# Kernel tuning notes

Hardware: AMD Instinct MI355X
Metric: run time of the kernel (lower is better)

Reference implementation:

```python
import jax, jax.numpy as jnp
import numpy as np

B, T, D = 8, 1024, 1024
H, HD, KVH, R = 16, 64, 4, 256   # heads, head_dim, kv_heads, kv_lora_rank
K = 31                            # depthwise conv kernel
FF = 4 * D
EPS = 1e-5


def _ln(x, g, b):
    m = jnp.mean(x, -1, keepdims=True)
    v = jnp.mean((x - m) ** 2, -1, keepdims=True)
    return (x - m) * jax.lax.rsqrt(v + EPS) * g + b


def _rope_tables(seq, dim):
    inv = 1.0 / (10000.0 ** (np.arange(0, dim, 2, dtype=np.float32) / dim))
    t = np.arange(seq, dtype=np.float32)
    f = np.einsum('i,j->ij', t, inv)
    emb = np.concatenate([f, f], -1)
    return jnp.asarray(np.cos(emb)), jnp.asarray(np.sin(emb))


def _rope(x, cos, sin):
    # x: [B, h, T, HD]; cos/sin: [T, HD]
    x1, x2 = jnp.split(x, 2, axis=-1)
    return x * cos + jnp.concatenate([-x2, x1], -1) * sin


def setup_inputs() -> dict:
    key = jax.random.key(0)
    ks = iter(jax.random.split(key, 48))
    def w(shape, s=0.02):
        return jax.random.normal(next(ks), shape, jnp.float32) * s
    d = {}
    d['x'] = jax.random.normal(next(ks), (B, T, D), jnp.float32)
    d['ff1_ng'] = jnp.ones(D); d['ff1_nb'] = jnp.zeros(D)
    d['ff1_w1'] = w((D, FF)); d['ff1_b1'] = jnp.zeros(FF)
    d['ff1_w2'] = w((FF, D)); d['ff1_b2'] = jnp.zeros(D)
    d['attn_ng'] = jnp.ones(D); d['attn_nb'] = jnp.zeros(D)
    d['wq'] = w((D, H * HD)); d['wkva'] = w((D, R + HD))
    d['kvn_g'] = jnp.ones(R); d['kvn_b'] = jnp.zeros(R)
    d['wkvb'] = w((R, KVH * HD * 2)); d['wo'] = w((H * HD, D))
    d['conv_ng'] = jnp.ones(D); d['conv_nb'] = jnp.zeros(D)
    d['pw1_w'] = w((D, 2 * D)); d['pw1_b'] = jnp.zeros(2 * D)
    d['dw_w'] = w((D, 1, K)); d['dw_b'] = jnp.zeros(D)
    d['bn_g'] = jnp.ones(D); d['bn_b'] = jnp.zeros(D)
    d['bn_rm'] = jnp.zeros(D); d['bn_rv'] = jnp.ones(D)
    d['pw2_w'] = w((D, D)); d['pw2_b'] = jnp.zeros(D)
    d['ff2_ng'] = jnp.ones(D); d['ff2_nb'] = jnp.zeros(D)
    d['ff2_w1'] = w((D, FF)); d['ff2_b1'] = jnp.zeros(FF)
    d['ff2_w2'] = w((FF, D)); d['ff2_b2'] = jnp.zeros(D)
    d['fin_g'] = jnp.ones(D); d['fin_b'] = jnp.zeros(D)
    return d


def _ffn(x, ng, nb, w1, b1, w2, b2):
    h = jax.nn.silu(_ln(x, ng, nb) @ w1 + b1)
    return h @ w2 + b2


def _rmla(x, ng, nb, wq, wkva, kvn_g, kvn_b, wkvb, wo):
    h = _ln(x, ng, nb)
    q = (h @ wq).reshape(B, T, H, HD).transpose(0, 2, 1, 3)
    kva = h @ wkva                                  # [B,T,R+HD]; k_pe part unused (as in source)
    lat = _ln(kva[..., :R], kvn_g, kvn_b)
    kv = lat @ wkvb
    k = kv[..., :KVH * HD].reshape(B, T, KVH, HD).transpose(0, 2, 1, 3)
    v = kv[..., KVH * HD:].reshape(B, T, KVH, HD).transpose(0, 2, 1, 3)
    cos, sin = _rope_tables(T, HD)
    q = _rope(q, cos, sin)
    k = _rope(k, cos, sin)
    g = H // KVH
    k = jnp.repeat(k, g, axis=1)
    v = jnp.repeat(v, g, axis=1)
    s = jnp.einsum('bhqd,bhkd->bhqk', q, k) * (HD ** -0.5)
    a = jax.nn.softmax(s.astype(jnp.float32), axis=-1).astype(q.dtype)
    o = jnp.einsum('bhqk,bhkd->bhqd', a, v)
    o = o.transpose(0, 2, 1, 3).reshape(B, T, H * HD)
    return o @ wo


def _convmod(x, ng, nb, pw1_w, pw1_b, dw_w, dw_b, bn_g, bn_b, bn_rm, bn_rv, pw2_w, pw2_b):
    h = _ln(x, ng, nb)
    h = h @ pw1_w + pw1_b                           # [B,T,2D]
    a, gate = jnp.split(h, 2, axis=-1)
    h = a * jax.nn.sigmoid(gate)                    # GLU over channels
    h = h.transpose(0, 2, 1)                        # [B,D,T]
    h = jax.lax.conv_general_dilated(h, dw_w, (1,), [(K // 2, K // 2)],
                                     dimension_numbers=('NCH', 'OIH', 'NCH'),
                                     feature_group_count=D) + dw_b[None, :, None]
    h = (h - bn_rm[None, :, None]) * jax.lax.rsqrt(bn_rv[None, :, None] + EPS)
    h = h * bn_g[None, :, None] + bn_b[None, :, None]
    h = jax.nn.silu(h)
    h = h.transpose(0, 2, 1)                        # [B,T,D]
    return h @ pw2_w + pw2_b


def reference(x, ff1_ng, ff1_nb, ff1_w1, ff1_b1, ff1_w2, ff1_b2,
              attn_ng, attn_nb, wq, wkva, kvn_g, kvn_b, wkvb, wo,
              conv_ng, conv_nb, pw1_w, pw1_b, dw_w, dw_b, bn_g, bn_b, bn_rm, bn_rv, pw2_w, pw2_b,
              ff2_ng, ff2_nb, ff2_w1, ff2_b1, ff2_w2, ff2_b2, fin_g, fin_b):
    # Conformer block (macaron): half-FF, RMLA attention, gated depthwise conv, half-FF, final LN
    x = x + 0.5 * _ffn(x, ff1_ng, ff1_nb, ff1_w1, ff1_b1, ff1_w2, ff1_b2)
    x = x + _rmla(x, attn_ng, attn_nb, wq, wkva, kvn_g, kvn_b, wkvb, wo)
    x = x + _convmod(x, conv_ng, conv_nb, pw1_w, pw1_b, dw_w, dw_b, bn_g, bn_b, bn_rm, bn_rv, pw2_w, pw2_b)
    x = x + 0.5 * _ffn(x, ff2_ng, ff2_nb, ff2_w1, ff2_b1, ff2_w2, ff2_b2)
    return _ln(x, fin_g, fin_b)
```

## Files before the change

### kernel.cpp

```cpp
#include <hip/hip_runtime.h>
#include <stdint.h>

typedef unsigned short u16;
using bf16x8 = __attribute__((ext_vector_type(8))) __bf16;
using f32x4  = __attribute__((ext_vector_type(4))) float;

__device__ __forceinline__ u16 f2bf(float f) {
    uint32_t u = __float_as_uint(f);
    u += 0x7fffu + ((u >> 16) & 1u);
    return (u16)(u >> 16);
}
__device__ __forceinline__ float bf2f(u16 u) {
    return __uint_as_float(((uint32_t)u) << 16);
}
__device__ __forceinline__ void gload16(const void* g, void* l) {
    __builtin_amdgcn_global_load_lds(
        (__attribute__((address_space(1))) void*)(uintptr_t)g,
        (__attribute__((address_space(3))) void*)(uintptr_t)l,
        16, 0, 0);
}

template <int OUTF32>
__global__ __launch_bounds__(256) void ln_kernel(const float* __restrict__ in,
                                                 const float* __restrict__ g,
                                                 const float* __restrict__ b,
                                                 void* __restrict__ out, int D) {
    const int row = blockIdx.x;
    const int tid = threadIdx.x;
    const float* x = in + (size_t)row * D;
    const int nv = D >> 8;
    float v[4];
    float s1 = 0.f, s2 = 0.f;
    for (int i = 0; i < nv; ++i) {
        float t = x[tid + (i << 8)];
        v[i] = t; s1 += t; s2 += t * t;
    }
    for (int o = 1; o < 64; o <<= 1) {
        s1 += __shfl_xor(s1, o, 64);
        s2 += __shfl_xor(s2, o, 64);
    }
    __shared__ float r1[4], r2[4];
    const int w = tid >> 6;
    if ((tid & 63) == 0) { r1[w] = s1; r2[w] = s2; }
    __syncthreads();
    s1 = r1[0] + r1[1] + r1[2] + r1[3];
    s2 = r2[0] + r2[1] + r2[2] + r2[3];
    const float mean = s1 / (float)D;
    const float var  = s2 / (float)D - mean * mean;
    const float inv  = rsqrtf(var + 1e-5f);
    for (int i = 0; i < nv; ++i) {
        int c = tid + (i << 8);
        float y = (v[i] - mean) * inv * g[c] + b[c];
        if (OUTF32) ((float*)out)[(size_t)row * D + c] = y;
        else        ((u16*)out)[(size_t)row * D + c] = f2bf(y);
    }
}

template <int GLUPERM>
__global__ __launch_bounds__(256) void wconvert_t(const float* __restrict__ W0,
                                                  u16* __restrict__ Wt0,
                                                  const float* __restrict__ W1,
                                                  u16* __restrict__ Wt1,
                                                  int K, int N, int ldw) {
    const float* W = blockIdx.z ? W1 : W0;
    u16* Wt = blockIdx.z ? Wt1 : Wt0;
    __shared__ float tile[32][33];
    const int k0 = blockIdx.x * 32, n0 = blockIdx.y * 32;
    const int tx = threadIdx.x & 31, ty = threadIdx.x >> 5;
    const int csrc = GLUPERM ? ((tx & 1) * 1024 + (n0 >> 1) + (tx >> 1)) : (n0 + tx);
    for (int i = 0; i < 4; ++i)
        tile[ty + i * 8][tx] = W[(size_t)(k0 + ty + i * 8) * ldw + csrc];
    __syncthreads();
    for (int i = 0; i < 4; ++i)
        Wt[(size_t)(n0 + ty + i * 8) * K + k0 + tx] = f2bf(tile[tx][ty + i * 8]);
}

template <int EPI, int WM>
__global__ __launch_bounds__(512, 2) void gemm256(const u16* __restrict__ A,
                                                  const u16* __restrict__ Bt,
                                                  const float* __restrict__ bias,
                                                  const float* __restrict__ res,
                                                  float rscale,
                                                  void* __restrict__ outp,
                                                  const float* __restrict__ CT,
                                                  const float* __restrict__ ST,
                                                  int M, int N, int K, int nbx) {
    constexpr int WN = 8 / WM;
    constexpr int BN = WN * 64;
    constexpr int FM = 16 / WM;
    __shared__ u16 sA[2][256 * 64];
    __shared__ u16 sB[2][BN * 64];
    const int tid = threadIdx.x, lane = tid & 63, w = tid >> 6;
    const int wm = w / WN, wn = w % WN;
    const int fr = lane & 15, fq = lane >> 4, frx = fr & 7;
    const int cpx = gridDim.x >> 3;
    const int lid = (blockIdx.x & 7) * cpx + (blockIdx.x >> 3);
    const int bn0 = (lid % nbx) * BN;
    const int bm0 = (lid / nbx) * 256;

    f32x4 acc[FM][4] = {};

    const int lrow = lane >> 3;
    const int lslot = (lane & 7) ^ (lrow & 7);
    const u16* ga = A  + (size_t)(bm0 + w * 8 + lrow) * K + lslot * 8;
    const u16* gb = Bt + (size_t)(bn0 + w * 8 + lrow) * K + lslot * 8;
    const size_t rs64 = (size_t)64 * K;
    const int lbase = w * 8 * 64;

    const int NK = K >> 6;

#define STAGE(bufi, kt)                                                        \
    {                                                                          \
        _Pragma("unroll")                                                      \
        for (int i = 0; i < 4; ++i)                                            \
            gload16(ga + (kt) + i * rs64, &sA[bufi][lbase + i * 4096]);        \
        _Pragma("unroll")                                                      \
        for (int i = 0; i < BN / 64; ++i)                                      \
            gload16(gb + (kt) + i * rs64, &sB[bufi][lbase + i * 4096]);        \
    }

    STAGE(0, 0)
    STAGE(1, 64)
    if constexpr (WM == 2) asm volatile("s_waitcnt vmcnt(8)" ::: "memory");
    else                   asm volatile("s_waitcnt vmcnt(6)" ::: "memory");
    __builtin_amdgcn_sched_barrier(0);
    __builtin_amdgcn_s_barrier();

    const int arow0 = wm * (256 / WM) + fr;
    const int brow0 = wn * 64 + fr;

    for (int s = 0; s < NK; ++s) {
        const int buf = s & 1;
        bf16x8 afr[FM], bfr[4];
#pragma unroll
        for (int mi = 0; mi < FM; ++mi)
            afr[mi] = *(const bf16x8*)(&sA[buf][(arow0 + mi * 16) * 64 + ((fq ^ frx) << 3)]);
#pragma unroll
        for (int ni = 0; ni < 4; ++ni)
            bfr[ni] = *(const bf16x8*)(&sB[buf][(brow0 + ni * 16) * 64 + ((fq ^ frx) << 3)]);
        asm volatile("s_waitcnt lgkmcnt(0)" ::: "memory");
        __builtin_amdgcn_sched_barrier(0);
        __builtin_amdgcn_s_setprio(1);
#pragma unroll
        for (int mi = 0; mi < FM; ++mi)
#pragma unroll
            for (int ni = 0; ni < 4; ++ni)
                acc[mi][ni] = __builtin_amdgcn_mfma_f32_16x16x32_bf16(
                    bfr[ni], afr[mi], acc[mi][ni], 0, 0, 0);
        __builtin_amdgcn_s_setprio(0);
#pragma unroll
        for (int mi = 0; mi < FM; ++mi)
            afr[mi] = *(const bf16x8*)(&sA[buf][(arow0 + mi * 16) * 64 + (((4 + fq) ^ frx) << 3)]);
#pragma unroll
        for (int ni = 0; ni < 4; ++ni)
            bfr[ni] = *(const bf16x8*)(&sB[buf][(brow0 + ni * 16) * 64 + (((4 + fq) ^ frx) << 3)]);
        asm volatile("s_waitcnt lgkmcnt(0)" ::: "memory");
        __builtin_amdgcn_sched_barrier(0);
        __builtin_amdgcn_s_barrier();
        if (s + 2 < NK) {
            STAGE(buf, (s + 2) << 6)
        }
        __builtin_amdgcn_sched_barrier(0);
        __builtin_amdgcn_s_setprio(1);
#pragma unroll
        for (int mi = 0; mi < FM; ++mi)
#pragma unroll
            for (int ni = 0; ni < 4; ++ni)
                acc[mi][ni] = __builtin_amdgcn_mfma_f32_16x16x32_bf16(
                    bfr[ni], afr[mi], acc[mi][ni], 0, 0, 0);
        __builtin_amdgcn_s_setprio(0);
        if (s + 2 < NK) {
            if constexpr (WM == 2) asm volatile("s_waitcnt vmcnt(8)" ::: "memory");
            else                   asm volatile("s_waitcnt vmcnt(6)" ::: "memory");
        } else {
            asm volatile("s_waitcnt vmcnt(0)" ::: "memory");
        }
        __builtin_amdgcn_sched_barrier(0);
        __builtin_amdgcn_s_barrier();
    }

#pragma unroll
    for (int mi = 0; mi < FM; ++mi) {
        const int m = bm0 + wm * (256 / WM) + mi * 16 + fr;
        if (EPI == 5) {
            const int tq = m & 1023;
            const int colbase = bn0 + wn * 64;
#pragma unroll
            for (int ni = 0; ni < 2; ++ni) {
                const int j0 = ni * 16 + fq * 4;
                const f32x4 c = *(const f32x4*)(CT + tq * 32 + j0);
                const f32x4 sn = *(const f32x4*)(ST + tq * 32 + j0);
                union { uint2 u2; u16 hh[4]; } o1, o2;
#pragma unroll
                for (int r = 0; r < 4; ++r) {
                    const float x1 = acc[mi][ni][r];
                    const float x2 = acc[mi][ni + 2][r];
                    o1.hh[r] = f2bf((x1 * c[r] - x2 * sn[r]) * rscale);
                    o2.hh[r] = f2bf((x2 * c[r] + x1 * sn[r]) * rscale);
                }
                *(uint2*)((u16*)outp + (size_t)m * N + colbase + j0) = o1.u2;
                *(uint2*)((u16*)outp + (size_t)m * N + colbase + j0 + 32) = o2.u2;
            }
            continue;
        }
#pragma unroll
        for (int ni = 0; ni < 4; ++ni) {
            const int n0 = bn0 + wn * 64 + ni * 16 + fq * 4;
            if (EPI == 0 || EPI == 1) {
                union { uint2 u2; u16 hh[4]; } ok;
#pragma unroll
                for (int r = 0; r < 4; ++r) {
                    float v = acc[mi][ni][r] + (bias ? bias[n0 + r] : 0.f);
                    if (EPI == 1) v = v / (1.f + __expf(-v));
                    ok.hh[r] = f2bf(v);
                }
                *(uint2*)((u16*)outp + (size_t)m * N + n0) = ok.u2;
            } else if (EPI == 3) {
                const f32x4 rv = *(const f32x4*)(res + (size_t)m * N + n0);
                f32x4 v;
#pragma unroll
                for (int r = 0; r < 4; ++r)
                    v[r] = rv[r] + rscale * (acc[mi][ni][r] + (bias ? bias[n0 + r] : 0.f));
                *(f32x4*)((float*)outp + (size_t)m * N + n0) = v;
            } else if (EPI == 4) {
                float vv[4];
#pragma unroll
                for (int r = 0; r < 4; ++r) {
                    const int n = n0 + r;
                    vv[r] = acc[mi][ni][r] + bias[((n & 1) << 10) + (n >> 1)];
                }
                union { uint32_t u; u16 hh[2]; } ok;
                ok.hh[0] = f2bf(vv[0] / (1.f + __expf(-vv[1])));
                ok.hh[1] = f2bf(vv[2] / (1.f + __expf(-vv[3])));
                *(uint32_t*)((u16*)outp + (size_t)m * (N >> 1) + (n0 >> 1)) = ok.u;
            }
        }
    }
#undef STAGE
}

template <int EPI>
__global__ __launch_bounds__(256, 2) void gemm128p(const u16* __restrict__ A,
                                                   const u16* __restrict__ Bt,
                                                   const float* __restrict__ bias,
                                                   const float* __restrict__ res,
                                                   float rscale,
                                                   void* __restrict__ outp,
                                                   const float* __restrict__ CT,
                                                   const float* __restrict__ ST,
                                                   int M, int N, int K, int nbx) {
    __shared__ u16 sA[2][128 * 64];
    __shared__ u16 sB[2][128 * 64];
    const int tid = threadIdx.x, lane = tid & 63, w = tid >> 6;
    const int wm = w >> 1, wn = w & 1;
    const int fr = lane & 15, fq = lane >> 4, frx = fr & 7;
    const int cpx = gridDim.x >> 3;
    const int lid = (blockIdx.x & 7) * cpx + (blockIdx.x >> 3);
    const int bn0 = (lid % nbx) * 128;
    const int bm0 = (lid / nbx) * 128;

    f32x4 acc[4][4] = {};

    const int lrow = lane >> 3;
    const int lslot = (lane & 7) ^ lrow;
    const u16* ga0 = A  + (size_t)(bm0 + w * 8 + lrow) * K + lslot * 8;
    const u16* gb0 = Bt + (size_t)(bn0 + w * 8 + lrow) * K + lslot * 8;
    const size_t rstep32 = (size_t)32 * K;
    const int NK = K >> 6;

#define STAGE(bufi, kt)                                                         \
    {                                                                           \
        _Pragma("unroll")                                                       \
        for (int i = 0; i < 4; ++i) {                                           \
            gload16(ga0 + (kt) + i * rstep32, &sA[bufi][w * 512 + i * 2048]);   \
            gload16(gb0 + (kt) + i * rstep32, &sB[bufi][w * 512 + i * 2048]);   \
        }                                                                       \
    }

    STAGE(0, 0)
    STAGE(1, 64)
    asm volatile("s_waitcnt vmcnt(8)" ::: "memory");
    __builtin_amdgcn_sched_barrier(0);
    __builtin_amdgcn_s_barrier();

    for (int s = 0; s < NK; ++s) {
        const int buf = s & 1;
        bf16x8 afr[4], bfr[4], afr2[4], bfr2[4];
#pragma unroll
        for (int i = 0; i < 4; ++i) {
            afr[i] = *(const bf16x8*)(&sA[buf][(wm * 64 + i * 16 + fr) * 64 + ((fq ^ frx) << 3)]);
            bfr[i] = *(const bf16x8*)(&sB[buf][(wn * 64 + i * 16 + fr) * 64 + ((fq ^ frx) << 3)]);
        }
        asm volatile("s_waitcnt lgkmcnt(0)" ::: "memory");
        __builtin_amdgcn_sched_barrier(0);
        __builtin_amdgcn_s_setprio(1);
#pragma unroll
        for (int mi = 0; mi < 4; ++mi)
#pragma unroll
            for (int ni = 0; ni < 4; ++ni)
                acc[mi][ni] = __builtin_amdgcn_mfma_f32_16x16x32_bf16(
                    bfr[ni], afr[mi], acc[mi][ni], 0, 0, 0);
        __builtin_amdgcn_s_setprio(0);
#pragma unroll
        for (int i = 0; i < 4; ++i) {
            afr2[i] = *(const bf16x8*)(&sA[buf][(wm * 64 + i * 16 + fr) * 64 + (((4 + fq) ^ frx) << 3)]);
            bfr2[i] = *(const bf16x8*)(&sB[buf][(wn * 64 + i * 16 + fr) * 64 + (((4 + fq) ^ frx) << 3)]);
        }
        asm volatile("s_waitcnt lgkmcnt(0)" ::: "memory");
        __builtin_amdgcn_sched_barrier(0);
        __builtin_amdgcn_s_barrier();
        if (s + 2 < NK) STAGE(buf, (s + 2) << 6)
        __builtin_amdgcn_sched_barrier(0);
        __builtin_amdgcn_s_setprio(1);
#pragma unroll
        for (int mi = 0; mi < 4; ++mi)
#pragma unroll
            for (int ni = 0; ni < 4; ++ni)
                acc[mi][ni] = __builtin_amdgcn_mfma_f32_16x16x32_bf16(
                    bfr2[ni], afr2[mi], acc[mi][ni], 0, 0, 0);
        __builtin_amdgcn_s_setprio(0);
        if (s + 2 < NK) { asm volatile("s_waitcnt vmcnt(8)" ::: "memory"); }
        else            { asm volatile("s_waitcnt vmcnt(0)" ::: "memory"); }
        __builtin_amdgcn_sched_barrier(0);
        __builtin_amdgcn_s_barrier();
    }

#pragma unroll
    for (int mi = 0; mi < 4; ++mi) {
        const int m = bm0 + wm * 64 + mi * 16 + fr;
        if (EPI == 6) {
            const int tq = m & 1023;
            const int colbase = bn0 + wn * 64;
            if (colbase < 256) {
#pragma unroll
                for (int ni = 0; ni < 2; ++ni) {
                    const int j0 = ni * 16 + fq * 4;
                    const f32x4 c = *(const f32x4*)(CT + tq * 32 + j0);
                    const f32x4 sn = *(const f32x4*)(ST + tq * 32 + j0);
                    union { uint2 u2; u16 hh[4]; } o1, o2;
#pragma unroll
                    for (int r = 0; r < 4; ++r) {
                        const float x1 = acc[mi][ni][r];
                        const float x2 = acc[mi][ni + 2][r];
                        o1.hh[r] = f2bf(x1 * c[r] - x2 * sn[r]);
                        o2.hh[r] = f2bf(x2 * c[r] + x1 * sn[r]);
                    }
                    *(uint2*)((u16*)outp + (size_t)m * N + colbase + j0) = o1.u2;
                    *(uint2*)((u16*)outp + (size_t)m * N + colbase + j0 + 32) = o2.u2;
                }
            } else {
#pragma unroll
                for (int ni = 0; ni < 4; ++ni) {
                    const int n0 = colbase + ni * 16 + fq * 4;
                    union { uint2 u2; u16 hh[4]; } ok;
#pragma unroll
                    for (int r = 0; r < 4; ++r) ok.hh[r] = f2bf(acc[mi][ni][r]);
                    *(uint2*)((u16*)outp + (size_t)m * N + n0) = ok.u2;
                }
            }
            continue;
        }
#pragma unroll
        for (int ni = 0; ni < 4; ++ni) {
            const int n0 = bn0 + wn * 64 + ni * 16 + fq * 4;
            f32x4 v;
#pragma unroll
            for (int r = 0; r < 4; ++r)
                v[r] = acc[mi][ni][r] + (bias ? bias[n0 + r] : 0.f);
            *(f32x4*)((float*)outp + (size_t)m * N + n0) = v;
        }
    }
#undef STAGE
}

__global__ __launch_bounds__(256) void rope_tables_kernel(float* __restrict__ ct,
                                                          float* __restrict__ st) {
    const int i = blockIdx.x * 256 + threadIdx.x;
    const int t = i >> 5, j = i & 31;
    const float inv = powf(10000.f, -(float)j / 32.f);
    const float f = (float)t * inv;
    ct[i] = cosf(f);
    st[i] = sinf(f);
}

__global__ __launch_bounds__(256) void vtranspose_kernel(const u16* __restrict__ KV,
                                                         u16* __restrict__ Vt) {
    __shared__ u16 tile[32][33];
    const int t0 = blockIdx.x * 32, h0 = blockIdx.y * 32;
    const int bk = blockIdx.z;
    const int b = bk >> 2, kh = bk & 3;
    const int tx = threadIdx.x & 31, ty = threadIdx.x >> 5;
    for (int i = 0; i < 4; ++i)
        tile[ty + i * 8][tx] =
            KV[(size_t)(b * 1024 + t0 + ty + i * 8) * 512 + 256 + kh * 64 + h0 + tx];
    __syncthreads();
    for (int i = 0; i < 4; ++i)
        Vt[((size_t)bk * 64 + h0 + ty + i * 8) * 1024 + t0 + tx] = tile[tx][ty + i * 8];
}

__global__ __launch_bounds__(256) void attn_kernel(const u16* __restrict__ Q,
                                                   const u16* __restrict__ KV,
                                                   const u16* __restrict__ Vt,
                                                   u16* __restrict__ O) {
    __shared__ __align__(16) u16 sK[2][64 * 64];
    __shared__ __align__(16) u16 sV[2][64 * 64];
    __shared__ __align__(16) u16 sP[4][16 * 64];
    const int tid = threadIdx.x, lane = tid & 63, w = tid >> 6;
    const int fr = lane & 15, fq = lane >> 4, frx = fr & 7;
    const int bk = blockIdx.x, b = bk >> 2, kh = bk & 3;
    const int h = kh * 4 + w;
    const int q0 = blockIdx.y * 16;
    const int qrow = b * 1024 + q0 + fr;

    const int srow = w * 16 + (lane >> 3);
    const int sslot = (lane & 7) ^ ((lane >> 3) & 7);
    const u16* gK = KV + (size_t)(b * 1024 + srow) * 512 + kh * 64 + sslot * 8;
    const u16* gV = Vt + (size_t)((b * 4 + kh) * 64 + srow) * 1024 + sslot * 8;
    u16* dK = (u16*)sK + w * 16 * 64;
    u16* dV = (u16*)sV + w * 16 * 64;

    bf16x8 qf[2];
    qf[0] = *(const bf16x8*)(Q + (size_t)qrow * 1024 + h * 64 + fq * 8);
    qf[1] = *(const bf16x8*)(Q + (size_t)qrow * 1024 + h * 64 + 32 + fq * 8);

    f32x4 oacc[4] = {};
    float mrun = -1e30f, lrun = 0.f;
    u16* sPw = sP[w];

    gload16(gK, dK);
    gload16(gK + (size_t)8 * 512, dK + 8 * 64);
    gload16(gV, dV);
    gload16(gV + (size_t)8 * 1024, dV + 8 * 64);
    __syncthreads();

    int cur = 0;
    for (int t = 0; t < 16; ++t) {
        const int kv0 = t * 64;
        if (t < 15) {
            const int kn = kv0 + 64;
            const int nx = (cur ^ 1) * 4096;
            gload16(gK + (size_t)kn * 512,       dK + nx);
            gload16(gK + (size_t)(kn + 8) * 512, dK + nx + 8 * 64);
            gload16(gV + kn,                     dV + nx);
            gload16(gV + kn + (size_t)8 * 1024,  dV + nx + 8 * 64);
        }
        const u16* sKc = (u16*)sK + cur * 4096;
        const u16* sVc = (u16*)sV + cur * 4096;
        f32x4 sacc[4] = {};
#pragma unroll
        for (int ks = 0; ks < 2; ++ks)
#pragma unroll
            for (int nb = 0; nb < 4; ++nb) {
                const bf16x8 kf = *(const bf16x8*)(
                    sKc + (nb * 16 + fr) * 64 + (((ks * 4 + fq) ^ frx) << 3));
                sacc[nb] = __builtin_amdgcn_mfma_f32_16x16x32_bf16(kf, qf[ks], sacc[nb], 0, 0, 0);
            }
        float pm;
        {
            float a0 = fmaxf(fmaxf(sacc[0][0], sacc[0][1]), fmaxf(sacc[0][2], sacc[0][3]));
            float a1 = fmaxf(fmaxf(sacc[1][0], sacc[1][1]), fmaxf(sacc[1][2], sacc[1][3]));
            float a2 = fmaxf(fmaxf(sacc[2][0], sacc[2][1]), fmaxf(sacc[2][2], sacc[2][3]));
            float a3 = fmaxf(fmaxf(sacc[3][0], sacc[3][1]), fmaxf(sacc[3][2], sacc[3][3]));
            pm = fmaxf(fmaxf(a0, a1), fmaxf(a2, a3));
        }
        pm = fmaxf(pm, __shfl_xor(pm, 16, 64));
        pm = fmaxf(pm, __shfl_xor(pm, 32, 64));
        if (!__all(pm <= mrun + 8.f)) {
            const float mn = fmaxf(mrun, pm);
            const float al = __expf(mrun - mn);
            mrun = mn;
            lrun *= al;
#pragma unroll
            for (int f = 0; f < 4; ++f) {
                f32x4 tt = oacc[f];
#pragma unroll
                for (int r = 0; r < 4; ++r) tt[r] *= al;
                oacc[f] = tt;
            }
        }
        float rs = 0.f;
#pragma unroll
        for (int nb = 0; nb < 4; ++nb) {
            union { uint2 u2; u16 hh[4]; } pk;
#pragma unroll
            for (int r = 0; r < 4; ++r) {
                const float p = __expf(sacc[nb][r] - mrun);
                rs += p;
                pk.hh[r] = f2bf(p);
            }
            const int slotl = nb * 2 + (fq >> 1);
            *(uint2*)(sPw + fr * 64 + (((slotl ^ frx) << 3) | ((fq & 1) << 2))) = pk.u2;
        }
        rs += __shfl_xor(rs, 16, 64);
        rs += __shfl_xor(rs, 32, 64);
        lrun += rs;
        asm volatile("s_waitcnt lgkmcnt(0)" ::: "memory");
        __builtin_amdgcn_sched_barrier(0);
#pragma unroll
        for (int ks2 = 0; ks2 < 2; ++ks2) {
            const bf16x8 pf = *(const bf16x8*)(
                sPw + fr * 64 + (((ks2 * 4 + fq) ^ frx) << 3));
#pragma unroll
            for (int f = 0; f < 4; ++f) {
                const bf16x8 vf = *(const bf16x8*)(
                    sVc + (f * 16 + fr) * 64 + (((ks2 * 4 + fq) ^ frx) << 3));
                oacc[f] = __builtin_amdgcn_mfma_f32_16x16x32_bf16(vf, pf, oacc[f], 0, 0, 0);
            }
        }
        __syncthreads();
        cur ^= 1;
    }

    const float linv = 1.f / lrun;
#pragma unroll
    for (int f = 0; f < 4; ++f) {
        union { uint2 u2; u16 hh[4]; } ok;
#pragma unroll
        for (int r = 0; r < 4; ++r) ok.hh[r] = f2bf(oacc[f][r] * linv);
        *(uint2*)(O + (size_t)qrow * 1024 + h * 64 + f * 16 + fq * 4) = ok.u2;
    }
}

__global__ __launch_bounds__(256) void dwconv_kernel(const u16* __restrict__ G,
                                                     const float* __restrict__ wt,
                                                     const float* __restrict__ wb,
                                                     const float* __restrict__ bg,
                                                     const float* __restrict__ bb,
                                                     const float* __restrict__ rm,
                                                     const float* __restrict__ rv,
                                                     u16* __restrict__ out) {
    __shared__ u16 sg[38 * 256];
    const int tid = threadIdx.x;
    const int d = blockIdx.x * 256 + tid;
    const int t0 = blockIdx.y * 8;
    const int b = blockIdx.z;
    const size_t base = (size_t)b * 1024 * 1024 + d;
    for (int i = 0; i < 38; ++i) {
        const int t = t0 - 15 + i;
        sg[i * 256 + tid] = (t >= 0 && t < 1024) ? G[base + (size_t)t * 1024] : (u16)0;
    }
    __syncthreads();
    float wreg[31];
#pragma unroll
    for (int k = 0; k < 31; ++k) wreg[k] = wt[d * 31 + k];
    const float scale = bg[d] * rsqrtf(rv[d] + 1e-5f);
    const float addv = wb[d] - rm[d];
#pragma unroll
    for (int j = 0; j < 8; ++j) {
        float acc = 0.f;
#pragma unroll
        for (int k = 0; k < 31; ++k) acc += bf2f(sg[(j + k) * 256 + tid]) * wreg[k];
        float y = (acc + addv) * scale + bb[d];
        y = y / (1.f + __expf(-y));
        out[base + (size_t)(t0 + j) * 1024] = f2bf(y);
    }
}

extern "C" void kernel_launch(void* const* d_in, const int* in_sizes, int n_in,
                              void* d_out, int out_size, void* d_ws, size_t ws_size,
                              hipStream_t stream) {
    (void)in_sizes; (void)n_in; (void)out_size;

    const float* x       = (const float*)d_in[0];
    const float* ff1_ng  = (const float*)d_in[1];
    const float* ff1_nb  = (const float*)d_in[2];
    const float* ff1_w1  = (const float*)d_in[3];
    const float* ff1_b1  = (const float*)d_in[4];
    const float* ff1_w2  = (const float*)d_in[5];
    const float* ff1_b2  = (const float*)d_in[6];
    const float* attn_ng = (const float*)d_in[7];
    const float* attn_nb = (const float*)d_in[8];
    const float* wq      = (const float*)d_in[9];
    const float* wkva    = (const float*)d_in[10];
    const float* kvn_g   = (const float*)d_in[11];
    const float* kvn_b   = (const float*)d_in[12];
    const float* wkvb    = (const float*)d_in[13];
    const float* wo      = (const float*)d_in[14];
    const float* conv_ng = (const float*)d_in[15];
    const float* conv_nb = (const float*)d_in[16];
    const float* pw1_w   = (const float*)d_in[17];
    const float* pw1_b   = (const float*)d_in[18];
    const float* dw_w    = (const float*)d_in[19];
    const float* dw_b    = (const float*)d_in[20];
    const float* bn_g    = (const float*)d_in[21];
    const float* bn_b    = (const float*)d_in[22];
    const float* bn_rm   = (const float*)d_in[23];
    const float* bn_rv   = (const float*)d_in[24];
    const float* pw2_w   = (const float*)d_in[25];
    const float* pw2_b   = (const float*)d_in[26];
    const float* ff2_ng  = (const float*)d_in[27];
    const float* ff2_nb  = (const float*)d_in[28];
    const float* ff2_w1  = (const float*)d_in[29];
    const float* ff2_b1  = (const float*)d_in[30];
    const float* ff2_w2  = (const float*)d_in[31];
    const float* ff2_b2  = (const float*)d_in[32];
    const float* fin_g   = (const float*)d_in[33];
    const float* fin_b   = (const float*)d_in[34];

    const int M = 8192;
    char* ws = (char*)d_ws;
    size_t off = 0;
    auto alloc = [&](size_t bytes) {
        size_t o = off;
        off += (bytes + 255) & ~(size_t)255;
        return o;
    };
    const size_t o_ff1w1 = alloc((size_t)4096 * 1024 * 2);
    const size_t o_ff1w2 = alloc((size_t)1024 * 4096 * 2);
    const size_t o_wq    = alloc((size_t)1024 * 1024 * 2);
    const size_t o_wkva  = alloc((size_t)256 * 1024 * 2);
    const size_t o_wkvb  = alloc((size_t)512 * 256 * 2);
    const size_t o_wo    = alloc((size_t)1024 * 1024 * 2);
    const size_t o_pw1   = alloc((size_t)2048 * 1024 * 2);
    const size_t o_pw2   = alloc((size_t)1024 * 1024 * 2);
    const size_t o_ff2w1 = alloc((size_t)4096 * 1024 * 2);
    const size_t o_ff2w2 = alloc((size_t)1024 * 4096 * 2);
    const size_t o_ctab  = alloc((size_t)1024 * 32 * 4);
    const size_t o_stab  = alloc((size_t)1024 * 32 * 4);
    const size_t o_xres  = alloc((size_t)M * 1024 * 4);
    const size_t o_ln    = alloc((size_t)M * 1024 * 2);
    const size_t o_bufa  = alloc((size_t)64 * 1024 * 1024);
    if (ws_size < off) return;

    u16* BUFA = (u16*)(ws + o_bufa);
    u16* Qb    = BUFA;
    u16* KVb   = (u16*)((char*)BUFA + (16u << 20));
    float* KVA = (float*)((char*)BUFA + (24u << 20));
    u16* LAT   = (u16*)((char*)BUFA + (32u << 20));
    u16* VT    = (u16*)((char*)BUFA + (36u << 20));
    u16* OB    = (u16*)((char*)BUFA + (40u << 20));
    u16* PW1G  = BUFA;
    u16* CONVO = (u16*)((char*)BUFA + (16u << 20));
    u16* HID   = BUFA;

    u16* WT_FF1W1 = (u16*)(ws + o_ff1w1);
    u16* WT_FF1W2 = (u16*)(ws + o_ff1w2);
    u16* WT_WQ    = (u16*)(ws + o_wq);
    u16* WT_WKVA  = (u16*)(ws + o_wkva);
    u16* WT_WKVB  = (u16*)(ws + o_wkvb);
    u16* WT_WO    = (u16*)(ws + o_wo);
    u16* WT_PW1   = (u16*)(ws + o_pw1);
    u16* WT_PW2   = (u16*)(ws + o_pw2);
    u16* WT_FF2W1 = (u16*)(ws + o_ff2w1);
    u16* WT_FF2W2 = (u16*)(ws + o_ff2w2);
    float* CT = (float*)(ws + o_ctab);
    float* ST = (float*)(ws + o_stab);
    float* XR = (float*)(ws + o_xres);
    u16* LNB  = (u16*)(ws + o_ln);

    wconvert_t<0><<<dim3(32, 128, 2), 256, 0, stream>>>(ff1_w1, WT_FF1W1, ff2_w1, WT_FF2W1, 1024, 4096, 4096);
    wconvert_t<0><<<dim3(128, 32, 2), 256, 0, stream>>>(ff1_w2, WT_FF1W2, ff2_w2, WT_FF2W2, 4096, 1024, 1024);
    wconvert_t<0><<<dim3(32, 32, 2),  256, 0, stream>>>(wq, WT_WQ, wo, WT_WO, 1024, 1024, 1024);
    wconvert_t<0><<<dim3(32, 32, 1),  256, 0, stream>>>(pw2_w, WT_PW2, pw2_w, WT_PW2, 1024, 1024, 1024);
    wconvert_t<0><<<dim3(32, 8, 1),   256, 0, stream>>>(wkva, WT_WKVA, wkva, WT_WKVA, 1024, 256, 320);
    wconvert_t<0><<<dim3(8, 16, 1),   256, 0, stream>>>(wkvb, WT_WKVB, wkvb, WT_WKVB, 256, 512, 512);
    wconvert_t<1><<<dim3(32, 64, 1),  256, 0, stream>>>(pw1_w, WT_PW1, pw1_w, WT_PW1, 1024, 2048, 2048);
    rope_tables_kernel<<<128, 256, 0, stream>>>(CT, ST);

    ln_kernel<0><<<M, 256, 0, stream>>>(x, ff1_ng, ff1_nb, LNB, 1024);
    gemm256<1, 2><<<512, 512, 0, stream>>>(LNB, WT_FF1W1, ff1_b1, nullptr, 0.f, HID, nullptr, nullptr, M, 4096, 1024, 16);
    gemm256<3, 4><<<256, 512, 0, stream>>>(HID, WT_FF1W2, ff1_b2, x, 0.5f, XR, nullptr, nullptr, M, 1024, 4096, 8);

    ln_kernel<0><<<M, 256, 0, stream>>>(XR, attn_ng, attn_nb, LNB, 1024);
    gemm256<5, 4><<<256, 512, 0, stream>>>(LNB, WT_WQ, nullptr, nullptr, 0.125f, Qb, CT, ST, M, 1024, 1024, 8);
    gemm128p<2><<<128, 256, 0, stream>>>(LNB, WT_WKVA, nullptr, nullptr, 0.f, KVA, nullptr, nullptr, M, 256, 1024, 2);
    ln_kernel<0><<<M, 256, 0, stream>>>(KVA, kvn_g, kvn_b, LAT, 256);
    gemm128p<6><<<256, 256, 0, stream>>>(LAT, WT_WKVB, nullptr, nullptr, 1.0f, KVb, CT, ST, M, 512, 256, 4);
    vtranspose_kernel<<<dim3(32, 2, 32), 256, 0, stream>>>(KVb, VT);
    attn_kernel<<<dim3(32, 64), 256, 0, stream>>>(Qb, KVb, VT, OB);
    gemm256<3, 4><<<256, 512, 0, stream>>>(OB, WT_WO, nullptr, XR, 1.f, XR, nullptr, nullptr, M, 1024, 1024, 8);

    ln_kernel<0><<<M, 256, 0, stream>>>(XR, conv_ng, conv_nb, LNB, 1024);
    gemm256<4, 2><<<256, 512, 0, stream>>>(LNB, WT_PW1, pw1_b, nullptr, 0.f, PW1G, nullptr, nullptr, M, 2048, 1024, 8);
    dwconv_kernel<<<dim3(4, 128, 8), 256, 0, stream>>>(PW1G, dw_w, dw_b, bn_g, bn_b, bn_rm, bn_rv, CONVO);
    gemm256<3, 4><<<256, 512, 0, stream>>>(CONVO, WT_PW2, pw2_b, XR, 1.f, XR, nullptr, nullptr, M, 1024, 1024, 8);

    ln_kernel<0><<<M, 256, 0, stream>>>(XR, ff2_ng, ff2_nb, LNB, 1024);
    gemm256<1, 2><<<512, 512, 0, stream>>>(LNB, WT_FF2W1, ff2_b1, nullptr, 0.f, HID, nullptr, nullptr, M, 4096, 1024, 16);
    gemm256<3, 4><<<256, 512, 0, stream>>>(HID, WT_FF2W2, ff2_b2, XR, 0.5f, XR, nullptr, nullptr, M, 1024, 4096, 8);

    ln_kernel<1><<<M, 256, 0, stream>>>(XR, fin_g, fin_b, d_out, 1024);
}
```

Before: 731.5 us.

## Replace 256-wide GEMM with 256x128 BK=32 triple-buffered kernel; vectorize LayerNorm

Replaces the templated gemm256 (BK=64, double-buffered, tile width depending on WM) with gemm32, which uses a fixed 256x128 tile, BK=32 and a three-stage LDS ring with a new swizzle. The prefetch is issued before the LDS reads, and the launch bound now targets 4 blocks per CU, aiming for more occupancy and better latency hiding. The cost is half as much work per barrier and less reuse per tile, with one barrier per 32-wide K step. LayerNorm also gets a D==1024 fast path that uses float4 loads and stores.

```diff
diff --git a/kernel.cpp b/kernel.cpp
--- a/kernel.cpp
+++ b/kernel.cpp
@@ -28,6 +28,38 @@
     const int row = blockIdx.x;
     const int tid = threadIdx.x;
     const float* x = in + (size_t)row * D;
+    __shared__ float r1[4], r2[4];
+    const int w = tid >> 6;
+    if (D == 1024) {
+        const f32x4 v = *(const f32x4*)(x + tid * 4);
+        float s1 = v[0] + v[1] + v[2] + v[3];
+        float s2 = v[0] * v[0] + v[1] * v[1] + v[2] * v[2] + v[3] * v[3];
+        for (int o = 1; o < 64; o <<= 1) {
+            s1 += __shfl_xor(s1, o, 64);
+            s2 += __shfl_xor(s2, o, 64);
+        }
+        if ((tid & 63) == 0) { r1[w] = s1; r2[w] = s2; }
+        __syncthreads();
+        s1 = r1[0] + r1[1] + r1[2] + r1[3];
+        s2 = r2[0] + r2[1] + r2[2] + r2[3];
+        const float mean = s1 * (1.f / 1024.f);
+        const float var  = s2 * (1.f / 1024.f) - mean * mean;
+        const float inv  = rsqrtf(var + 1e-5f);
+        const f32x4 gg = *(const f32x4*)(g + tid * 4);
+        const f32x4 bb = *(const f32x4*)(b + tid * 4);
+        if (OUTF32) {
+            f32x4 y;
+#pragma unroll
+            for (int r = 0; r < 4; ++r) y[r] = (v[r] - mean) * inv * gg[r] + bb[r];
+            *(f32x4*)((float*)out + (size_t)row * 1024 + tid * 4) = y;
+        } else {
+            union { uint2 u2; u16 hh[4]; } ok;
+#pragma unroll
+            for (int r = 0; r < 4; ++r) ok.hh[r] = f2bf((v[r] - mean) * inv * gg[r] + bb[r]);
+            *(uint2*)((u16*)out + (size_t)row * 1024 + tid * 4) = ok.u2;
+        }
+        return;
+    }
     const int nv = D >> 8;
     float v[4];
     float s1 = 0.f, s2 = 0.f;
@@ -39,8 +71,6 @@
         s1 += __shfl_xor(s1, o, 64);
         s2 += __shfl_xor(s2, o, 64);
     }
-    __shared__ float r1[4], r2[4];
-    const int w = tid >> 6;
     if ((tid & 63) == 0) { r1[w] = s1; r2[w] = s2; }
     __syncthreads();
     s1 = r1[0] + r1[1] + r1[2] + r1[3];
@@ -75,113 +105,87 @@
         Wt[(size_t)(n0 + ty + i * 8) * K + k0 + tx] = f2bf(tile[tx][ty + i * 8]);
 }
 
-template <int EPI, int WM>
-__global__ __launch_bounds__(512, 2) void gemm256(const u16* __restrict__ A,
-                                                  const u16* __restrict__ Bt,
-                                                  const float* __restrict__ bias,
-                                                  const float* __restrict__ res,
-                                                  float rscale,
-                                                  void* __restrict__ outp,
-                                                  const float* __restrict__ CT,
-                                                  const float* __restrict__ ST,
-                                                  int M, int N, int K, int nbx) {
-    constexpr int WN = 8 / WM;
-    constexpr int BN = WN * 64;
-    constexpr int FM = 16 / WM;
-    __shared__ u16 sA[2][256 * 64];
-    __shared__ u16 sB[2][BN * 64];
+template <int EPI>
+__global__ __launch_bounds__(512, 4) void gemm32(const u16* __restrict__ A,
+                                                 const u16* __restrict__ Bt,
+                                                 const float* __restrict__ bias,
+                                                 const float* __restrict__ res,
+                                                 float rscale,
+                                                 void* __restrict__ outp,
+                                                 const float* __restrict__ CT,
+                                                 const float* __restrict__ ST,
+                                                 int M, int N, int K, int nbx) {
+    __shared__ u16 sA[3][256 * 32];
+    __shared__ u16 sB[3][128 * 32];
     const int tid = threadIdx.x, lane = tid & 63, w = tid >> 6;
-    const int wm = w / WN, wn = w % WN;
-    const int fr = lane & 15, fq = lane >> 4, frx = fr & 7;
+    const int wm = w >> 1, wn = w & 1;
+    const int fr = lane & 15, fq = lane >> 4;
     const int cpx = gridDim.x >> 3;
     const int lid = (blockIdx.x & 7) * cpx + (blockIdx.x >> 3);
-    const int bn0 = (lid % nbx) * BN;
+    const int bn0 = (lid % nbx) * 128;
     const int bm0 = (lid / nbx) * 256;
 
-    f32x4 acc[FM][4] = {};
-
-    const int lrow = lane >> 3;
-    const int lslot = (lane & 7) ^ (lrow & 7);
-    const u16* ga = A  + (size_t)(bm0 + w * 8 + lrow) * K + lslot * 8;
-    const u16* gb = Bt + (size_t)(bn0 + w * 8 + lrow) * K + lslot * 8;
-    const size_t rs64 = (size_t)64 * K;
-    const int lbase = w * 8 * 64;
-
-    const int NK = K >> 6;
-
-#define STAGE(bufi, kt)                                                        \
-    {                                                                          \
-        _Pragma("unroll")                                                      \
-        for (int i = 0; i < 4; ++i)                                            \
-            gload16(ga + (kt) + i * rs64, &sA[bufi][lbase + i * 4096]);        \
-        _Pragma("unroll")                                                      \
-        for (int i = 0; i < BN / 64; ++i)                                      \
-            gload16(gb + (kt) + i * rs64, &sB[bufi][lbase + i * 4096]);        \
-    }
+    f32x4 acc[4][4] = {};
+
+    const int lr = lane >> 2;
+    const int sg = (lane & 3) ^ ((lane >> 3) & 3);
+    const u16* ga = A  + (size_t)(bm0 + w * 16 + lr) * K + sg * 8;
+    const u16* gb = Bt + (size_t)(bn0 + w * 16 + lr) * K + sg * 8;
+    const size_t rs128 = (size_t)128 * K;
+    const int lbase = w * 512;
+
+    const int NK = K >> 5;
+    const int rdsl = (fq ^ ((fr >> 1) & 3)) << 3;
+    const int arow0 = wm * 64 + fr;
+    const int brow0 = wn * 64 + fr;
+
+#define STAGE(bufi, s)                                                   \
+    {                                                                    \
+        gload16(ga + ((s) << 5),         &sA[bufi][lbase]);              \
+        gload16(ga + ((s) << 5) + rs128, &sA[bufi][lbase + 4096]);       \
+        gload16(gb + ((s) << 5),         &sB[bufi][lbase]);              \
+    }
+#define SB() __builtin_amdgcn_sched_barrier(0)
 
     STAGE(0, 0)
-    STAGE(1, 64)
-    if constexpr (WM == 2) asm volatile("s_waitcnt vmcnt(8)" ::: "memory");
-    else                   asm volatile("s_waitcnt vmcnt(6)" ::: "memory");
-    __builtin_amdgcn_sched_barrier(0);
+    STAGE(1, 1)
+    asm volatile("s_waitcnt vmcnt(3)" ::: "memory");
+    SB();
     __builtin_amdgcn_s_barrier();
 
-    const int arow0 = wm * (256 / WM) + fr;
-    const int brow0 = wn * 64 + fr;
-
+    int buf = 0;
     for (int s = 0; s < NK; ++s) {
-        const int buf = s & 1;
-        bf16x8 afr[FM], bfr[4];
-#pragma unroll
-        for (int mi = 0; mi < FM; ++mi)
-            afr[mi] = *(const bf16x8*)(&sA[buf][(arow0 + mi * 16) * 64 + ((fq ^ frx) << 3)]);
-#pragma unroll
-        for (int ni = 0; ni < 4; ++ni)
-            bfr[ni] = *(const bf16x8*)(&sB[buf][(brow0 + ni * 16) * 64 + ((fq ^ frx) << 3)]);
+        if (s + 2 < NK) {
+            int bn = buf + 2;
+            if (bn >= 3) bn -= 3;
+            STAGE(bn, s + 2)
+        }
+        bf16x8 afr[4], bfr[4];
+#pragma unroll
+        for (int i = 0; i < 4; ++i) {
+            afr[i] = *(const bf16x8*)(&sA[buf][(arow0 + i * 16) * 32 + rdsl]);
+            bfr[i] = *(const bf16x8*)(&sB[buf][(brow0 + i * 16) * 32 + rdsl]);
+        }
         asm volatile("s_waitcnt lgkmcnt(0)" ::: "memory");
-        __builtin_amdgcn_sched_barrier(0);
+        SB();
         __builtin_amdgcn_s_setprio(1);
 #pragma unroll
-        for (int mi = 0; mi < FM; ++mi)
+        for (int mi = 0; mi < 4; ++mi)
 #pragma unroll
             for (int ni = 0; ni < 4; ++ni)
                 acc[mi][ni] = __builtin_amdgcn_mfma_f32_16x16x32_bf16(
                     bfr[ni], afr[mi], acc[mi][ni], 0, 0, 0);
         __builtin_amdgcn_s_setprio(0);
-#pragma unroll
-        for (int mi = 0; mi < FM; ++mi)
-            afr[mi] = *(const bf16x8*)(&sA[buf][(arow0 + mi * 16) * 64 + (((4 + fq) ^ frx) << 3)]);
-#pragma unroll
-        for (int ni = 0; ni < 4; ++ni)
-            bfr[ni] = *(const bf16x8*)(&sB[buf][(brow0 + ni * 16) * 64 + (((4 + fq) ^ frx) << 3)]);
-        asm volatile("s_waitcnt lgkmcnt(0)" ::: "memory");
-        __builtin_amdgcn_sched_barrier(0);
+        if (s + 2 < NK)      { asm volatile("s_waitcnt vmcnt(3)" ::: "memory"); }
+        else if (s + 1 < NK) { asm volatile("s_waitcnt vmcnt(0)" ::: "memory"); }
+        SB();
         __builtin_amdgcn_s_barrier();
-        if (s + 2 < NK) {
-            STAGE(buf, (s + 2) << 6)
-        }
-        __builtin_amdgcn_sched_barrier(0);
-        __builtin_amdgcn_s_setprio(1);
-#pragma unroll
-        for (int mi = 0; mi < FM; ++mi)
-#pragma unroll
-            for (int ni = 0; ni < 4; ++ni)
-                acc[mi][ni] = __builtin_amdgcn_mfma_f32_16x16x32_bf16(
-                    bfr[ni], afr[mi], acc[mi][ni], 0, 0, 0);
-        __builtin_amdgcn_s_setprio(0);
-        if (s + 2 < NK) {
-            if constexpr (WM == 2) asm volatile("s_waitcnt vmcnt(8)" ::: "memory");
-            else                   asm volatile("s_waitcnt vmcnt(6)" ::: "memory");
-        } else {
-            asm volatile("s_waitcnt vmcnt(0)" ::: "memory");
-        }
-        __builtin_amdgcn_sched_barrier(0);
-        __builtin_amdgcn_s_barrier();
-    }
-
-#pragma unroll
-    for (int mi = 0; mi < FM; ++mi) {
-        const int m = bm0 + wm * (256 / WM) + mi * 16 + fr;
+        buf = (buf == 2) ? 0 : buf + 1;
+    }
+
+#pragma unroll
+    for (int mi = 0; mi < 4; ++mi) {
+        const int m = bm0 + wm * 64 + mi * 16 + fr;
         if (EPI == 5) {
             const int tq = m & 1023;
             const int colbase = bn0 + wn * 64;
@@ -237,6 +241,7 @@
         }
     }
 #undef STAGE
+#undef SB
 }
 
 template <int EPI>
@@ -658,26 +663,26 @@
     rope_tables_kernel<<<128, 256, 0, stream>>>(CT, ST);
 
     ln_kernel<0><<<M, 256, 0, stream>>>(x, ff1_ng, ff1_nb, LNB, 1024);
-    gemm256<1, 2><<<512, 512, 0, stream>>>(LNB, WT_FF1W1, ff1_b1, nullptr, 0.f, HID, nullptr, nullptr, M, 4096, 1024, 16);
-    gemm256<3, 4><<<256, 512, 0, stream>>>(HID, WT_FF1W2, ff1_b2, x, 0.5f, XR, nullptr, nullptr, M, 1024, 4096, 8);
+    gemm32<1><<<1024, 512, 0, stream>>>(LNB, WT_FF1W1, ff1_b1, nullptr, 0.f, HID, nullptr, nullptr, M, 4096, 1024, 32);
+    gemm32<3><<<256, 512, 0, stream>>>(HID, WT_FF1W2, ff1_b2, x, 0.5f, XR, nullptr, nullptr, M, 1024, 4096, 8);
 
     ln_kernel<0><<<M, 256, 0, stream>>>(XR, attn_ng, attn_nb, LNB, 1024);
-    gemm256<5, 4><<<256, 512, 0, stream>>>(LNB, WT_WQ, nullptr, nullptr, 0.125f, Qb, CT, ST, M, 1024, 1024, 8);
+    gemm32<5><<<256, 512, 0, stream>>>(LNB, WT_WQ, nullptr, nullptr, 0.125f, Qb, CT, ST, M, 1024, 1024, 8);
     gemm128p<2><<<128, 256, 0, stream>>>(LNB, WT_WKVA, nullptr, nullptr, 0.f, KVA, nullptr, nullptr, M, 256, 1024, 2);
     ln_kernel<0><<<M, 256, 0, stream>>>(KVA, kvn_g, kvn_b, LAT, 256);
     gemm128p<6><<<256, 256, 0, stream>>>(LAT, WT_WKVB, nullptr, nullptr, 1.0f, KVb, CT, ST, M, 512, 256, 4);
     vtranspose_kernel<<<dim3(32, 2, 32), 256, 0, stream>>>(KVb, VT);
     attn_kernel<<<dim3(32, 64), 256, 0, stream>>>(Qb, KVb, VT, OB);
-    gemm256<3, 4><<<256, 512, 0, stream>>>(OB, WT_WO, nullptr, XR, 1.f, XR, nullptr, nullptr, M, 1024, 1024, 8);
+    gemm32<3><<<256, 512, 0, stream>>>(OB, WT_WO, nullptr, XR, 1.f, XR, nullptr, nullptr, M, 1024, 1024, 8);
 
     ln_kernel<0><<<M, 256, 0, stream>>>(XR, conv_ng, conv_nb, LNB, 1024);
-    gemm256<4, 2><<<256, 512, 0, stream>>>(LNB, WT_PW1, pw1_b, nullptr, 0.f, PW1G, nullptr, nullptr, M, 2048, 1024, 8);
+    gemm32<4><<<512, 512, 0, stream>>>(LNB, WT_PW1, pw1_b, nullptr, 0.f, PW1G, nullptr, nullptr, M, 2048, 1024, 16);
     dwconv_kernel<<<dim3(4, 128, 8), 256, 0, stream>>>(PW1G, dw_w, dw_b, bn_g, bn_b, bn_rm, bn_rv, CONVO);
-    gemm256<3, 4><<<256, 512, 0, stream>>>(CONVO, WT_PW2, pw2_b, XR, 1.f, XR, nullptr, nullptr, M, 1024, 1024, 8);
+    gemm32<3><<<256, 512, 0, stream>>>(CONVO, WT_PW2, pw2_b, XR, 1.f, XR, nullptr, nullptr, M, 1024, 1024, 8);
 
     ln_kernel<0><<<M, 256, 0, stream>>>(XR, ff2_ng, ff2_nb, LNB, 1024);
-    gemm256<1, 2><<<512, 512, 0, stream>>>(LNB, WT_FF2W1, ff2_b1, nullptr, 0.f, HID, nullptr, nullptr, M, 4096, 1024, 16);
-    gemm256<3, 4><<<256, 512, 0, stream>>>(HID, WT_FF2W2, ff2_b2, XR, 0.5f, XR, nullptr, nullptr, M, 1024, 4096, 8);
+    gemm32<1><<<1024, 512, 0, stream>>>(LNB, WT_FF2W1, ff2_b1, nullptr, 0.f, HID, nullptr, nullptr, M, 4096, 1024, 32);
+    gemm32<3><<<256, 512, 0, stream>>>(HID, WT_FF2W2, ff2_b2, XR, 0.5f, XR, nullptr, nullptr, M, 1024, 4096, 8);
 
     ln_kernel<1><<<M, 256, 0, stream>>>(XR, fin_g, fin_b, d_out, 1024);
 }
```

Result: faster. 712.1 us (-2.7%).
